# Kernel optimization log

Measured on AMD Instinct MI355X. Metric: run time of the kernel, lower is better.

## Reference

```python
import jax, jax.numpy as jnp
import numpy as np

N_NODES = 100000
N_EDGES = 600000
IN_C = 128


def setup_inputs() -> dict:
    key = jax.random.key(0)
    ks = jax.random.split(key, 10)
    x = jax.random.normal(ks[0], (N_NODES, IN_C), dtype=jnp.float32)
    edge_index = jax.random.randint(ks[1], (2, N_EDGES), 0, N_NODES, dtype=jnp.int64)
    edge_weight = jax.random.uniform(ks[2], (N_EDGES,), dtype=jnp.float32)
    s = 1.0 / np.sqrt(IN_C)
    # EvolveGCNO initial GCN weight [in, in]
    W0 = jax.random.uniform(ks[3], (IN_C, IN_C), minval=-s, maxval=s, dtype=jnp.float32)
    # GRU(input=in, hidden=in) params, gate order (r, z, n)
    W_ih = jax.random.uniform(ks[4], (3 * IN_C, IN_C), minval=-s, maxval=s, dtype=jnp.float32)
    W_hh = jax.random.uniform(ks[5], (3 * IN_C, IN_C), minval=-s, maxval=s, dtype=jnp.float32)
    b_ih = jax.random.uniform(ks[6], (3 * IN_C,), minval=-s, maxval=s, dtype=jnp.float32)
    b_hh = jax.random.uniform(ks[7], (3 * IN_C,), minval=-s, maxval=s, dtype=jnp.float32)
    cls_w = jax.random.uniform(ks[8], (1, IN_C), minval=-s, maxval=s, dtype=jnp.float32)
    cls_b = jax.random.uniform(ks[9], (1,), minval=-s, maxval=s, dtype=jnp.float32)
    return {"x": x, "edge_index": edge_index, "edge_weight": edge_weight,
            "W0": W0, "W_ih": W_ih, "W_hh": W_hh, "b_ih": b_ih, "b_hh": b_hh,
            "cls_w": cls_w, "cls_b": cls_b}


def reference(x, edge_index, edge_weight, W0, W_ih, W_hh, b_ih, b_hh, cls_w, cls_b):
    n = x.shape[0]
    # --- EvolveGCNO: GRU step with input = hidden = W0 (batch = in_channels rows) ---
    gi = W0 @ W_ih.T + b_ih
    gh = W0 @ W_hh.T + b_hh
    i_r, i_z, i_n = jnp.split(gi, 3, axis=1)
    h_r, h_z, h_n = jnp.split(gh, 3, axis=1)
    r = jax.nn.sigmoid(i_r + h_r)
    z = jax.nn.sigmoid(i_z + h_z)
    cand = jnp.tanh(i_n + r * h_n)
    W = (1.0 - z) * cand + z * W0  # evolved GCN weight [in, in]
    # --- GCNConv with fixed W: add self-loops, symmetric normalization ---
    loops = jnp.arange(n, dtype=edge_index.dtype)
    row = jnp.concatenate([edge_index[0], loops])  # source
    col = jnp.concatenate([edge_index[1], loops])  # target
    w = jnp.concatenate([edge_weight, jnp.ones((n,), x.dtype)])
    deg = jax.ops.segment_sum(w, col, num_segments=n)
    dinv = jnp.where(deg > 0, jax.lax.rsqrt(jnp.maximum(deg, 1e-30)), 0.0)
    norm = dinv[row] * w * dinv[col]  # [E+N]
    h = x @ W  # [N, in]
    agg = jax.ops.segment_sum(norm[:, None] * h[row], col, num_segments=n)  # [N, in]
    # --- ReLU + linear classifier ---
    h = jax.nn.relu(agg)
    return h @ cls_w.T + cls_b  # [N, 1]
```

## Files before the change

kernel.cpp:

```cpp
#include <hip/hip_runtime.h>
#include <math.h>

#define IN_C 128
#define CAP 32

typedef short short8 __attribute__((ext_vector_type(8)));
typedef float floatx4 __attribute__((ext_vector_type(4)));
typedef unsigned long long u64;

static __device__ __forceinline__ unsigned short f2bf(float f) {
    unsigned int u = __float_as_uint(f);
    u += 0x7fffu + ((u >> 16) & 1u);
    return (unsigned short)(u >> 16);
}

__global__ __launch_bounds__(256) void zero_evolve(
        const float* __restrict__ W0, const float* __restrict__ Wih,
        const float* __restrict__ Whh, const float* __restrict__ bih,
        const float* __restrict__ bhh, unsigned short* __restrict__ Wbt,
        u64* __restrict__ pk, int n, int ZB) {
    const int b = blockIdx.x;
    const int t = threadIdx.x;
    if (b < 64) {
        __shared__ float w0row[2][IN_C];
        const int r2 = t >> 7;
        const int j = t & 127;
        const int i = b * 2 + r2;
        w0row[r2][j] = W0[i * IN_C + j];
        __syncthreads();
        float ir = bih[j], iz = bih[j + IN_C], inn = bih[j + 2 * IN_C];
        float hr = bhh[j], hz = bhh[j + IN_C], hnn = bhh[j + 2 * IN_C];
        const float* wr = &Wih[(size_t)j * IN_C];
        const float* wz = &Wih[(size_t)(j + IN_C) * IN_C];
        const float* wn = &Wih[(size_t)(j + 2 * IN_C) * IN_C];
        const float* ur = &Whh[(size_t)j * IN_C];
        const float* uz = &Whh[(size_t)(j + IN_C) * IN_C];
        const float* un = &Whh[(size_t)(j + 2 * IN_C) * IN_C];
        #pragma unroll 4
        for (int k = 0; k < IN_C; ++k) {
            const float a = w0row[r2][k];
            ir = fmaf(a, wr[k], ir); iz = fmaf(a, wz[k], iz); inn = fmaf(a, wn[k], inn);
            hr = fmaf(a, ur[k], hr); hz = fmaf(a, uz[k], hz); hnn = fmaf(a, un[k], hnn);
        }
        const float r = 1.0f / (1.0f + expf(-(ir + hr)));
        const float z = 1.0f / (1.0f + expf(-(iz + hz)));
        const float cand = tanhf(inn + r * hnn);
        Wbt[j * IN_C + i] = f2bf((1.0f - z) * cand + z * w0row[r2][j]);
    } else {
        const int stride = ZB * 256;
        for (int i = (b - 64) * 256 + t; i < n; i += stride) pk[i] = 0ull;
    }
}

#define ALD 136
__global__ __launch_bounds__(256) void hist_place_gemm(
        const int* __restrict__ rowi, const int* __restrict__ coli,
        const float* __restrict__ ew,
        u64* __restrict__ pk, u64* __restrict__ edge_cap, int E, int EB, int M,
        const float* __restrict__ x, const unsigned short* __restrict__ Wbt,
        unsigned short* __restrict__ hb, int n) {
    __shared__ unsigned short As[128 * ALD];
    __shared__ unsigned short Ws[128 * ALD];
    const int i = blockIdx.x;
    const int t = threadIdx.x;
    const int prev = (int)(((long long)i * EB) / M);
    const int next = (int)(((long long)(i + 1) * EB) / M);

    if (next > prev) {
        const int e0 = (prev * 256 + t) * 4;
        if (e0 + 3 < E) {
            const int4 r4 = *(const int4*)&rowi[e0];
            const int4 c4 = *(const int4*)&coli[e0];
            const float4 w4 = *(const float4*)&ew[e0];
            const u64 o0 = atomicAdd(&pk[c4.x], (1ull << 32) | (u64)(unsigned int)(w4.x * 16777216.0f));
            const u64 o1 = atomicAdd(&pk[c4.y], (1ull << 32) | (u64)(unsigned int)(w4.y * 16777216.0f));
            const u64 o2 = atomicAdd(&pk[c4.z], (1ull << 32) | (u64)(unsigned int)(w4.z * 16777216.0f));
            const u64 o3 = atomicAdd(&pk[c4.w], (1ull << 32) | (u64)(unsigned int)(w4.w * 16777216.0f));
            const unsigned int k0 = (unsigned int)(o0 >> 32);
            const unsigned int k1 = (unsigned int)(o1 >> 32);
            const unsigned int k2 = (unsigned int)(o2 >> 32);
            const unsigned int k3 = (unsigned int)(o3 >> 32);
            if (k0 < CAP) edge_cap[(size_t)c4.x * CAP + k0] = (u64)(unsigned)r4.x | ((u64)__float_as_uint(w4.x) << 32);
            if (k1 < CAP) edge_cap[(size_t)c4.y * CAP + k1] = (u64)(unsigned)r4.y | ((u64)__float_as_uint(w4.y) << 32);
            if (k2 < CAP) edge_cap[(size_t)c4.z * CAP + k2] = (u64)(unsigned)r4.z | ((u64)__float_as_uint(w4.z) << 32);
            if (k3 < CAP) edge_cap[(size_t)c4.w * CAP + k3] = (u64)(unsigned)r4.w | ((u64)__float_as_uint(w4.w) << 32);
        } else {
            for (int e = e0; e < E; ++e) {
                const u64 o = atomicAdd(&pk[coli[e]],
                    (1ull << 32) | (u64)(unsigned int)(ew[e] * 16777216.0f));
                const unsigned int rk = (unsigned int)(o >> 32);
                if (rk < CAP)
                    edge_cap[(size_t)coli[e] * CAP + rk] = (u64)(unsigned)rowi[e] | ((u64)__float_as_uint(ew[e]) << 32);
            }
        }
        return;
    }

    const size_t row0 = (size_t)(i - prev) * 128;

    for (int idx = t; idx < 2048; idx += 256) {
        const int nn = idx >> 4, k8 = (idx & 15) * 8;
        *(uint4*)&Ws[nn * ALD + k8] = *(const uint4*)&Wbt[nn * IN_C + k8];
    }
    for (int idx = t; idx < 4096; idx += 256) {
        const int r = idx >> 5, c4 = (idx & 31) * 4;
        size_t row = row0 + r;
        if (row >= (size_t)n) row = (size_t)n - 1;
        const float4 v = *(const float4*)&x[row * IN_C + c4];
        ushort4 bb;
        bb.x = f2bf(v.x); bb.y = f2bf(v.y); bb.z = f2bf(v.z); bb.w = f2bf(v.w);
        *(ushort4*)&As[r * ALD + c4] = bb;
    }
    __syncthreads();

    const int w = t >> 6, lane = t & 63, ln = lane & 15, quad = lane >> 4;
    floatx4 acc[2][8];
    #pragma unroll
    for (int mt = 0; mt < 2; ++mt)
        #pragma unroll
        for (int nt = 0; nt < 8; ++nt)
            acc[mt][nt] = (floatx4){0.f, 0.f, 0.f, 0.f};

    #pragma unroll
    for (int k0 = 0; k0 < 128; k0 += 32) {
        const short8 a0 = *(const short8*)&As[(w * 32 + ln) * ALD + k0 + quad * 8];
        const short8 a1 = *(const short8*)&As[(w * 32 + 16 + ln) * ALD + k0 + quad * 8];
        #pragma unroll
        for (int nt = 0; nt < 8; ++nt) {
            const short8 bb = *(const short8*)&Ws[(nt * 16 + ln) * ALD + k0 + quad * 8];
            acc[0][nt] = __builtin_amdgcn_mfma_f32_16x16x32_bf16(a0, bb, acc[0][nt], 0, 0, 0);
            acc[1][nt] = __builtin_amdgcn_mfma_f32_16x16x32_bf16(a1, bb, acc[1][nt], 0, 0, 0);
        }
    }

    #pragma unroll
    for (int mt = 0; mt < 2; ++mt) {
        #pragma unroll
        for (int reg = 0; reg < 4; ++reg) {
            const size_t row = row0 + w * 32 + mt * 16 + quad * 4 + reg;
            if (row < (size_t)n) {
                #pragma unroll
                for (int nt = 0; nt < 8; ++nt)
                    hb[row * IN_C + nt * 16 + ln] = f2bf(acc[mt][nt][reg]);
            }
        }
    }
}

__global__ __launch_bounds__(256) void gather_classify(
        const unsigned short* __restrict__ hb, const u64* __restrict__ pk,
        const u64* __restrict__ edge_cap,
        const float* __restrict__ cls_w, const float* __restrict__ cls_b,
        float* __restrict__ out, int n) {
    const int wid = __builtin_amdgcn_readfirstlane((blockIdx.x * blockDim.x + threadIdx.x) >> 6);
    const int lane = threadIdx.x & 63;
    if (wid >= n) return;

    const u64 pv = pk[wid];
    int cnt = (int)(pv >> 32);
    if (cnt > CAP) cnt = CAP;
    const float dvc = rsqrtf((float)(unsigned int)(pv & 0xffffffffull) * (1.0f / 16777216.0f) + 1.0f);

    unsigned int hv = *(const unsigned int*)&hb[(size_t)wid * IN_C + 2 * lane];
    float ax = dvc * dvc * __uint_as_float(hv << 16);
    float ay = dvc * dvc * __uint_as_float(hv & 0xffff0000u);

    const size_t ebase = (size_t)wid * CAP;
    for (int e = 0; e < cnt; e += 8) {
        u64 p[8];
        #pragma unroll
        for (int i = 0; i < 8; ++i) {
            const int idx = (e + i < cnt) ? (e + i) : (cnt - 1);
            p[i] = edge_cap[ebase + idx];
        }
        u64 q[8];
        unsigned int hr[8];
        #pragma unroll
        for (int i = 0; i < 8; ++i) {
            const unsigned int src = (unsigned int)(p[i] & 0xffffffffull);
            q[i] = pk[src];
            hr[i] = *(const unsigned int*)&hb[(size_t)src * IN_C + 2 * lane];
        }
        #pragma unroll
        for (int i = 0; i < 8; ++i) {
            const float dvs = rsqrtf((float)(unsigned int)(q[i] & 0xffffffffull) * (1.0f / 16777216.0f) + 1.0f);
            const float wgt = __uint_as_float((unsigned int)(p[i] >> 32));
            const float nm = (e + i < cnt) ? wgt * dvs * dvc : 0.0f;
            ax = fmaf(nm, __uint_as_float(hr[i] << 16), ax);
            ay = fmaf(nm, __uint_as_float(hr[i] & 0xffff0000u), ay);
        }
    }

    const float2 wv = *(const float2*)&cls_w[2 * lane];
    float sum = wv.x * fmaxf(ax, 0.0f) + wv.y * fmaxf(ay, 0.0f);
    #pragma unroll
    for (int off = 32; off > 0; off >>= 1) sum += __shfl_down(sum, off);
    if (lane == 0) out[wid] = sum + cls_b[0];
}

extern "C" void kernel_launch(void* const* d_in, const int* in_sizes, int n_in,
                              void* d_out, int out_size, void* d_ws, size_t ws_size,
                              hipStream_t stream) {
    const float* x    = (const float*)d_in[0];
    const int*   eidx = (const int*)d_in[1];
    const float* ew   = (const float*)d_in[2];
    const float* W0   = (const float*)d_in[3];
    const float* Wih  = (const float*)d_in[4];
    const float* Whh  = (const float*)d_in[5];
    const float* bih  = (const float*)d_in[6];
    const float* bhh  = (const float*)d_in[7];
    const float* clsw = (const float*)d_in[8];
    const float* clsb = (const float*)d_in[9];
    float* out = (float*)d_out;

    const int n = in_sizes[0] / IN_C;
    const int E = in_sizes[2];
    const int* rowi = eidx;
    const int* coli = eidx + E;

    u64* pk = (u64*)d_ws;
    u64* edge_cap = pk + n;
    unsigned short* Wbt = (unsigned short*)(edge_cap + (size_t)n * CAP);
    unsigned short* hb  = Wbt + 16384;

    const int EB = (E + 1023) / 1024;
    const int GB = (n + 127) / 128;
    const int M = EB + GB;
    const int ZB = 128;

    zero_evolve<<<dim3(64 + ZB), dim3(256), 0, stream>>>(W0, Wih, Whh, bih, bhh, Wbt, pk, n, ZB);
    hist_place_gemm<<<dim3(M), dim3(256), 0, stream>>>(rowi, coli, ew, pk, edge_cap, E, EB, M,
                                                       x, Wbt, hb, n);
    gather_classify<<<dim3((n + 3) / 4), dim3(256), 0, stream>>>(hb, pk, edge_cap,
                                                                 clsw, clsb, out, n);
}
```

Baseline: 216.8 us.

## Zero edge capacity buffer and process two nodes per wavefront in gather

The gather kernel now assigns two nodes per 64-lane wavefront, with each half-wave lane handling four channels through 8-byte loads. The first 8 capacity slots are loaded unconditionally, which is safe because the zero kernel now clears the whole pk+edge_cap region, so empty slots carry zero weight. The dvc scaling is also factored out of the inner loop. This adds zero-fill traffic for the edge_cap buffer (n*CAP u64) and doubles the zeroing grid, in exchange for fewer per-edge branches and better lane utilisation.

```diff
diff --git a/kernel.cpp b/kernel.cpp
--- a/kernel.cpp
+++ b/kernel.cpp
@@ -47,8 +47,11 @@
         const float cand = tanhf(inn + r * hnn);
         Wbt[j * IN_C + i] = f2bf((1.0f - z) * cand + z * w0row[r2][j]);
     } else {
-        const int stride = ZB * 256;
-        for (int i = (b - 64) * 256 + t; i < n; i += stride) pk[i] = 0ull;
+        uint4* z = (uint4*)pk;
+        const size_t nquad = ((size_t)n * (CAP + 1)) >> 1;
+        const uint4 zero4 = make_uint4(0u, 0u, 0u, 0u);
+        const size_t stride = (size_t)ZB * 256;
+        for (size_t i = (size_t)(b - 64) * 256 + t; i < nquad; i += stride) z[i] = zero4;
     }
 }
 
@@ -152,50 +155,85 @@
         const u64* __restrict__ edge_cap,
         const float* __restrict__ cls_w, const float* __restrict__ cls_b,
         float* __restrict__ out, int n) {
-    const int wid = __builtin_amdgcn_readfirstlane((blockIdx.x * blockDim.x + threadIdx.x) >> 6);
+    const int gwid = (blockIdx.x * blockDim.x + threadIdx.x) >> 6;
     const int lane = threadIdx.x & 63;
-    if (wid >= n) return;
-
-    const u64 pv = pk[wid];
+    const int half = lane >> 5;
+    const int sl = lane & 31;
+    const int nid = gwid * 2 + half;
+    if (nid >= n) return;
+
+    const int ch0 = sl * 4;
+    const size_t ebase = (size_t)nid * CAP;
+
+    const u64 pv = pk[nid];
+    const uint2 hs = *(const uint2*)&hb[(size_t)nid * IN_C + ch0];
+    u64 p[8];
+    #pragma unroll
+    for (int i = 0; i < 8; ++i) p[i] = edge_cap[ebase + i];
+
+    float s0 = 0.f, s1 = 0.f, s2 = 0.f, s3 = 0.f;
+
+    {
+        u64 q[8];
+        uint2 hr[8];
+        #pragma unroll
+        for (int i = 0; i < 8; ++i) {
+            const unsigned int src = (unsigned int)p[i];
+            q[i] = pk[src];
+            hr[i] = *(const uint2*)&hb[(size_t)src * IN_C + ch0];
+        }
+        #pragma unroll
+        for (int i = 0; i < 8; ++i) {
+            const float w = __uint_as_float((unsigned int)(p[i] >> 32));
+            const float dvs = rsqrtf((float)(unsigned int)q[i] * (1.0f / 16777216.0f) + 1.0f);
+            const float nm = w * dvs;
+            s0 = fmaf(nm, __uint_as_float(hr[i].x << 16), s0);
+            s1 = fmaf(nm, __uint_as_float(hr[i].x & 0xffff0000u), s1);
+            s2 = fmaf(nm, __uint_as_float(hr[i].y << 16), s2);
+            s3 = fmaf(nm, __uint_as_float(hr[i].y & 0xffff0000u), s3);
+        }
+    }
+
     int cnt = (int)(pv >> 32);
     if (cnt > CAP) cnt = CAP;
-    const float dvc = rsqrtf((float)(unsigned int)(pv & 0xffffffffull) * (1.0f / 16777216.0f) + 1.0f);
-
-    unsigned int hv = *(const unsigned int*)&hb[(size_t)wid * IN_C + 2 * lane];
-    float ax = dvc * dvc * __uint_as_float(hv << 16);
-    float ay = dvc * dvc * __uint_as_float(hv & 0xffff0000u);
-
-    const size_t ebase = (size_t)wid * CAP;
-    for (int e = 0; e < cnt; e += 8) {
-        u64 p[8];
+    for (int e = 8; e < cnt; e += 8) {
+        u64 p2[8];
         #pragma unroll
         for (int i = 0; i < 8; ++i) {
             const int idx = (e + i < cnt) ? (e + i) : (cnt - 1);
-            p[i] = edge_cap[ebase + idx];
+            p2[i] = edge_cap[ebase + idx];
         }
         u64 q[8];
-        unsigned int hr[8];
-        #pragma unroll
-        for (int i = 0; i < 8; ++i) {
-            const unsigned int src = (unsigned int)(p[i] & 0xffffffffull);
+        uint2 hr[8];
+        #pragma unroll
+        for (int i = 0; i < 8; ++i) {
+            const unsigned int src = (unsigned int)p2[i];
             q[i] = pk[src];
-            hr[i] = *(const unsigned int*)&hb[(size_t)src * IN_C + 2 * lane];
-        }
-        #pragma unroll
-        for (int i = 0; i < 8; ++i) {
-            const float dvs = rsqrtf((float)(unsigned int)(q[i] & 0xffffffffull) * (1.0f / 16777216.0f) + 1.0f);
-            const float wgt = __uint_as_float((unsigned int)(p[i] >> 32));
-            const float nm = (e + i < cnt) ? wgt * dvs * dvc : 0.0f;
-            ax = fmaf(nm, __uint_as_float(hr[i] << 16), ax);
-            ay = fmaf(nm, __uint_as_float(hr[i] & 0xffff0000u), ay);
-        }
-    }
-
-    const float2 wv = *(const float2*)&cls_w[2 * lane];
-    float sum = wv.x * fmaxf(ax, 0.0f) + wv.y * fmaxf(ay, 0.0f);
-    #pragma unroll
-    for (int off = 32; off > 0; off >>= 1) sum += __shfl_down(sum, off);
-    if (lane == 0) out[wid] = sum + cls_b[0];
+            hr[i] = *(const uint2*)&hb[(size_t)src * IN_C + ch0];
+        }
+        #pragma unroll
+        for (int i = 0; i < 8; ++i) {
+            const float w = __uint_as_float((unsigned int)(p2[i] >> 32));
+            const float dvs = rsqrtf((float)(unsigned int)q[i] * (1.0f / 16777216.0f) + 1.0f);
+            const float nm = (e + i < cnt) ? w * dvs : 0.0f;
+            s0 = fmaf(nm, __uint_as_float(hr[i].x << 16), s0);
+            s1 = fmaf(nm, __uint_as_float(hr[i].x & 0xffff0000u), s1);
+            s2 = fmaf(nm, __uint_as_float(hr[i].y << 16), s2);
+            s3 = fmaf(nm, __uint_as_float(hr[i].y & 0xffff0000u), s3);
+        }
+    }
+
+    const float dvc = rsqrtf((float)(unsigned int)pv * (1.0f / 16777216.0f) + 1.0f);
+    const float4 wv = *(const float4*)&cls_w[ch0];
+    const float a0 = dvc * fmaf(dvc, __uint_as_float(hs.x << 16), s0);
+    const float a1 = dvc * fmaf(dvc, __uint_as_float(hs.x & 0xffff0000u), s1);
+    const float a2 = dvc * fmaf(dvc, __uint_as_float(hs.y << 16), s2);
+    const float a3 = dvc * fmaf(dvc, __uint_as_float(hs.y & 0xffff0000u), s3);
+    float sum = wv.x * fmaxf(a0, 0.f) + wv.y * fmaxf(a1, 0.f)
+              + wv.z * fmaxf(a2, 0.f) + wv.w * fmaxf(a3, 0.f);
+    #pragma unroll
+    for (int off = 16; off > 0; off >>= 1) sum += __shfl_down(sum, off);
+    if (sl == 0) out[nid] = sum + cls_b[0];
 }
 
 extern "C" void kernel_launch(void* const* d_in, const int* in_sizes, int n_in,
@@ -226,11 +264,12 @@
     const int EB = (E + 1023) / 1024;
     const int GB = (n + 127) / 128;
     const int M = EB + GB;
-    const int ZB = 128;
+    const int ZB = 256;
 
     zero_evolve<<<dim3(64 + ZB), dim3(256), 0, stream>>>(W0, Wih, Whh, bih, bhh, Wbt, pk, n, ZB);
     hist_place_gemm<<<dim3(M), dim3(256), 0, stream>>>(rowi, coli, ew, pk, edge_cap, E, EB, M,
                                                        x, Wbt, hb, n);
-    gather_classify<<<dim3((n + 3) / 4), dim3(256), 0, stream>>>(hb, pk, edge_cap,
-                                                                 clsw, clsb, out, n);
-}
+    const int waves = (n + 1) / 2;
+    gather_classify<<<dim3((waves + 3) / 4), dim3(256), 0, stream>>>(hb, pk, edge_cap,
+                                                                     clsw, clsb, out, n);
+}
```

Result: faster. 208.0 us (-4.1%).
